# Kernel tuning notes

Measured on AMD Instinct MI355X. Metric: run time of the kernel, lower is better.

## Reference

```python
import jax, jax.numpy as jnp
import numpy as np

VOCAB = 50257
CH = 1024          # c_hidden_size = hidden_size(1020) + class_num(4)
LAT = 128
T = 1024
EOS = 1


def setup_inputs() -> dict:
    key = jax.random.key(0)
    ks = jax.random.split(key, 12)
    s = 0.02
    # tokens in [2, VOCAB) so EOS only appears at the final position
    toks = jax.random.randint(ks[0], (T,), 2, VOCAB, dtype=jnp.int32)
    input_tensor = toks.at[-1].set(EOS)
    inp = {
        "input_tensor": input_tensor,
        "h0": jnp.zeros((1, 1, CH), jnp.float32),
        "c0": jnp.zeros((1, 1, CH), jnp.float32),
        "eps": jax.random.normal(ks[1], (1, 1, LAT), jnp.float32),
        "emb": jax.random.normal(ks[2], (VOCAB, CH), jnp.float32) * s,
        "W_ih": jax.random.normal(ks[3], (4 * CH, CH), jnp.float32) * s,
        "W_hh": jax.random.normal(ks[4], (4 * CH, CH), jnp.float32) * s,
        "b_ih": jax.random.normal(ks[5], (4 * CH,), jnp.float32) * s,
        "b_hh": jax.random.normal(ks[6], (4 * CH,), jnp.float32) * s,
        "W_mean": jax.random.normal(ks[7], (LAT, 2 * CH), jnp.float32) * s,
        "b_mean": jnp.zeros((LAT,), jnp.float32),
        "W_logv": jax.random.normal(ks[8], (LAT, 2 * CH), jnp.float32) * s,
        "b_logv": jnp.zeros((LAT,), jnp.float32),
    }
    return inp


def reference(input_tensor, h0, c0, eps, emb, W_ih, W_hh, b_ih, b_hh,
              W_mean, b_mean, W_logv, b_logv):
    Tlen = input_tensor.shape[0]
    eos_idx = jnp.argmax(input_tensor == EOS)           # first EOS position
    active = jnp.arange(Tlen) < eos_idx                 # steps taken before break
    x_all = emb[input_tensor]                            # [T, CH]

    def step(carry, inp):
        h, c = carry
        x, a = inp
        gates = x @ W_ih.T + b_ih + h @ W_hh.T + b_hh    # [4*CH]
        i, f, g, o = jnp.split(gates, 4)                 # PyTorch LSTM gate order
        c_new = jax.nn.sigmoid(f) * c + jax.nn.sigmoid(i) * jnp.tanh(g)
        h_new = jax.nn.sigmoid(o) * jnp.tanh(c_new)
        h = jnp.where(a, h_new, h)
        c = jnp.where(a, c_new, c)
        return (h, c), None

    (h, c), _ = jax.lax.scan(step, (h0.reshape(-1), c0.reshape(-1)), (x_all, active))
    hc = jnp.concatenate([h, c])                         # cat((h, c), dim=2) flattened
    mean = hc @ W_mean.T + b_mean
    logv = hc @ W_logv.T + b_logv
    z = eps.reshape(-1) * jnp.exp(0.5 * logv) + mean     # reparameterize
    shp = (1, 1, LAT)
    return z.reshape(shp), mean.reshape(shp), logv.reshape(shp)
```

## Files before the change

kernel.cpp:

```cpp
#include <hip/hip_runtime.h>
#include <cstdint>
#include <cstddef>

#define T_LEN 1024
#define CH    1024
#define NGATE 4096
#define LAT   128
#define NBLK  128

#define WS_XG    0
#define WS_HBUF  (16777216)
#define WS_HFIN  (16777216 + 16384)
#define WS_CFIN  (16777216 + 24576)
#define WS_CTRL  (16777216 + 32768)

#define SWZ(i) ((i) ^ ((((i) >> 4) & 7) << 2))

__device__ __forceinline__ float sigmf(float x) { return 1.0f / (1.0f + expf(-x)); }

template <int CTRL, int RM>
__device__ __forceinline__ float dpp_add(float x) {
  int t = __builtin_amdgcn_update_dpp(0, __float_as_int(x), CTRL, RM, 0xf, true);
  return x + __int_as_float(t);
}

__device__ __forceinline__ float wave_sum63(float x) {
  x = dpp_add<0x111, 0xf>(x);
  x = dpp_add<0x112, 0xf>(x);
  x = dpp_add<0x114, 0xf>(x);
  x = dpp_add<0x118, 0xf>(x);
  x = dpp_add<0x142, 0xa>(x);
  x = dpp_add<0x143, 0xc>(x);
  return x;
}

__global__ __launch_bounds__(1024) void setup_k(const int* __restrict__ tok,
                                                int* __restrict__ ctrl) {
  __shared__ int red[1024];
  int tid = threadIdx.x;
  red[tid] = (tok[tid] == 1) ? tid : 0x7fffffff;
  __syncthreads();
  for (int s = 512; s > 0; s >>= 1) {
    if (tid < s) red[tid] = min(red[tid], red[tid + s]);
    __syncthreads();
  }
  if (tid == 0) {
    int e = red[0];
    ctrl[0] = (e == 0x7fffffff) ? 0 : e;
  }
}

__global__ __launch_bounds__(512) void xgemm_k(const int* __restrict__ tok,
                                               const float* __restrict__ emb,
                                               const float* __restrict__ Wih,
                                               const float* __restrict__ bih,
                                               const float* __restrict__ bhh,
                                               float* __restrict__ xg) {
  __shared__ float As[16 * 132];
  __shared__ float Bs[16 * 132];
  const int tid = threadIdx.x;
  const int r0 = blockIdx.x * 128;
  const int t0 = blockIdx.y * 128;
  const int tx = tid & 15, ty = tid >> 4;
  const int m0 = ty * 4, n0 = tx * 8;
  const int lrow = tid >> 2;
  const int kq   = (tid & 3) * 4;

  float acc[4][8];
#pragma unroll
  for (int i = 0; i < 4; i++)
#pragma unroll
    for (int j = 0; j < 8; j++) acc[i][j] = 0.0f;

  const int tokv = tok[t0 + lrow];
  const float* arow = emb + (size_t)tokv * CH;
  const float* brow = Wih + (size_t)(r0 + lrow) * CH;

  for (int k0 = 0; k0 < CH; k0 += 16) {
    float4 a4 = *(const float4*)(arow + k0 + kq);
    float4 b4 = *(const float4*)(brow + k0 + kq);
    __syncthreads();
    As[(kq + 0) * 132 + lrow] = a4.x;
    As[(kq + 1) * 132 + lrow] = a4.y;
    As[(kq + 2) * 132 + lrow] = a4.z;
    As[(kq + 3) * 132 + lrow] = a4.w;
    Bs[(kq + 0) * 132 + lrow] = b4.x;
    Bs[(kq + 1) * 132 + lrow] = b4.y;
    Bs[(kq + 2) * 132 + lrow] = b4.z;
    Bs[(kq + 3) * 132 + lrow] = b4.w;
    __syncthreads();
#pragma unroll
    for (int kk = 0; kk < 16; kk++) {
      float4 av = *(const float4*)&As[kk * 132 + m0];
      float4 b0 = *(const float4*)&Bs[kk * 132 + n0];
      float4 b1 = *(const float4*)&Bs[kk * 132 + n0 + 4];
      float aa[4] = {av.x, av.y, av.z, av.w};
      float bb[8] = {b0.x, b0.y, b0.z, b0.w, b1.x, b1.y, b1.z, b1.w};
#pragma unroll
      for (int i = 0; i < 4; i++)
#pragma unroll
        for (int j = 0; j < 8; j++) acc[i][j] += aa[i] * bb[j];
    }
  }

  float4 bi0 = *(const float4*)(bih + r0 + n0);
  float4 bi1 = *(const float4*)(bih + r0 + n0 + 4);
  float4 bh0 = *(const float4*)(bhh + r0 + n0);
  float4 bh1 = *(const float4*)(bhh + r0 + n0 + 4);
  float badd[8] = {bi0.x + bh0.x, bi0.y + bh0.y, bi0.z + bh0.z, bi0.w + bh0.w,
                   bi1.x + bh1.x, bi1.y + bh1.y, bi1.z + bh1.z, bi1.w + bh1.w};
#pragma unroll
  for (int i = 0; i < 4; i++) {
    float4 o0 = {acc[i][0] + badd[0], acc[i][1] + badd[1],
                 acc[i][2] + badd[2], acc[i][3] + badd[3]};
    float4 o1 = {acc[i][4] + badd[4], acc[i][5] + badd[5],
                 acc[i][6] + badd[6], acc[i][7] + badd[7]};
    float* dst = xg + (size_t)(t0 + m0 + i) * NGATE + r0 + n0;
    *(float4*)(dst) = o0;
    *(float4*)(dst + 4) = o1;
  }
}

__global__ __launch_bounds__(1024) void lstm_k(const float* __restrict__ h0,
                                               const float* __restrict__ c0,
                                               const float* __restrict__ eps,
                                               const float* __restrict__ Whh,
                                               const float* __restrict__ Wm,
                                               const float* __restrict__ bm,
                                               const float* __restrict__ Wl,
                                               const float* __restrict__ bl,
                                               const float* __restrict__ xg,
                                               unsigned long long* __restrict__ hbuf64,
                                               unsigned long long* __restrict__ hfin64,
                                               unsigned long long* __restrict__ cfin64,
                                               const int* __restrict__ ctrl,
                                               float* __restrict__ out) {
  __shared__ float hs[1024];
  __shared__ float hcs[2048];
  __shared__ float4 gpart[16];
  __shared__ float rs[32];

  const int tid = threadIdx.x;
  const int b = blockIdx.x;
  const int wv = tid >> 6;
  const int ln = tid & 63;
  const int dw = wv & 7;
  const int mb = (wv >> 3) * 2;
  const int hsw = SWZ(tid);
  const int swzmask = (ln & 7) << 2;
  const int idx0 = (ln * 16 + 4 * mb) ^ swzmask;
  const int idx1 = (ln * 16 + 4 * mb + 4) ^ swzmask;

  float4 w4[4][2];
#pragma unroll
  for (int q = 0; q < 4; q++) {
    const float* wr = Whh + (size_t)(q * 1024 + b * 8 + dw) * CH + ln * 16 + 4 * mb;
    w4[q][0] = *(const float4*)(wr);
    w4[q][1] = *(const float4*)(wr + 4);
  }

  const int eos = ctrl[0];

  float hreg = 0.0f, creg = 0.0f;
  if (tid < 8) { hreg = h0[b * 8 + tid]; creg = c0[b * 8 + tid]; }

  for (int t = 0; t < eos; t++) {
    float xq0 = 0.0f, xq1 = 0.0f, xq2 = 0.0f, xq3 = 0.0f;
    if (tid < 8) {
      const float* xp = xg + (size_t)t * NGATE + b * 8 + tid;
      xq0 = xp[0]; xq1 = xp[1024]; xq2 = xp[2048]; xq3 = xp[3072];
    }

    if (t == 0) {
      hs[hsw] = h0[tid];
    } else {
      const unsigned want = (unsigned)t;
      const unsigned long long* src = hbuf64 + (size_t)(t & 1) * 1024 + tid;
      unsigned long long v;
      do {
        v = __hip_atomic_load(src, __ATOMIC_RELAXED, __HIP_MEMORY_SCOPE_AGENT);
      } while ((unsigned)(v >> 32) != want);
      hs[hsw] = __uint_as_float((unsigned)(v & 0xffffffffu));
    }
    __syncthreads();

    float a0 = 0.0f, a1 = 0.0f, a2 = 0.0f, a3 = 0.0f;
    {
      const float4 h4a = *(const float4*)&hs[idx0];
      const float4 h4b = *(const float4*)&hs[idx1];
      a0 += w4[0][0].x * h4a.x; a0 += w4[0][0].y * h4a.y;
      a0 += w4[0][0].z * h4a.z; a0 += w4[0][0].w * h4a.w;
      a0 += w4[0][1].x * h4b.x; a0 += w4[0][1].y * h4b.y;
      a0 += w4[0][1].z * h4b.z; a0 += w4[0][1].w * h4b.w;
      a1 += w4[1][0].x * h4a.x; a1 += w4[1][0].y * h4a.y;
      a1 += w4[1][0].z * h4a.z; a1 += w4[1][0].w * h4a.w;
      a1 += w4[1][1].x * h4b.x; a1 += w4[1][1].y * h4b.y;
      a1 += w4[1][1].z * h4b.z; a1 += w4[1][1].w * h4b.w;
      a2 += w4[2][0].x * h4a.x; a2 += w4[2][0].y * h4a.y;
      a2 += w4[2][0].z * h4a.z; a2 += w4[2][0].w * h4a.w;
      a2 += w4[2][1].x * h4b.x; a2 += w4[2][1].y * h4b.y;
      a2 += w4[2][1].z * h4b.z; a2 += w4[2][1].w * h4b.w;
      a3 += w4[3][0].x * h4a.x; a3 += w4[3][0].y * h4a.y;
      a3 += w4[3][0].z * h4a.z; a3 += w4[3][0].w * h4a.w;
      a3 += w4[3][1].x * h4b.x; a3 += w4[3][1].y * h4b.y;
      a3 += w4[3][1].z * h4b.z; a3 += w4[3][1].w * h4b.w;
    }
    a0 = wave_sum63(a0);
    a1 = wave_sum63(a1);
    a2 = wave_sum63(a2);
    a3 = wave_sum63(a3);
    if (ln == 63) gpart[wv] = float4{a0, a1, a2, a3};
    __syncthreads();

    if (tid < 8) {
      const float4 g0 = gpart[tid];
      const float4 g1 = gpart[tid + 8];
      const float iv = g0.x + g1.x + xq0;
      const float fv = g0.y + g1.y + xq1;
      const float gg = g0.z + g1.z + xq2;
      const float ov = g0.w + g1.w + xq3;
      const float cn = sigmf(fv) * creg + sigmf(iv) * tanhf(gg);
      const float hn = sigmf(ov) * tanhf(cn);
      creg = cn; hreg = hn;
      const unsigned long long pv =
          ((unsigned long long)(unsigned)(t + 1) << 32) |
          (unsigned long long)__float_as_uint(hn);
      __hip_atomic_store(&hbuf64[(size_t)((t + 1) & 1) * 1024 + b * 8 + tid], pv,
                         __ATOMIC_RELAXED, __HIP_MEMORY_SCOPE_AGENT);
    }
  }

  if (tid < 8) {
    const unsigned long long ph = (1ull << 32) | (unsigned long long)__float_as_uint(hreg);
    const unsigned long long pc = (1ull << 32) | (unsigned long long)__float_as_uint(creg);
    __hip_atomic_store(&hfin64[b * 8 + tid], ph, __ATOMIC_RELAXED, __HIP_MEMORY_SCOPE_AGENT);
    __hip_atomic_store(&cfin64[b * 8 + tid], pc, __ATOMIC_RELAXED, __HIP_MEMORY_SCOPE_AGENT);
  }

  {
    unsigned long long vh, vc;
    do {
      vh = __hip_atomic_load(&hfin64[tid], __ATOMIC_RELAXED, __HIP_MEMORY_SCOPE_AGENT);
    } while ((unsigned)(vh >> 32) != 1u);
    do {
      vc = __hip_atomic_load(&cfin64[tid], __ATOMIC_RELAXED, __HIP_MEMORY_SCOPE_AGENT);
    } while ((unsigned)(vc >> 32) != 1u);
    hcs[tid] = __uint_as_float((unsigned)(vh & 0xffffffffu));
    hcs[1024 + tid] = __uint_as_float((unsigned)(vc & 0xffffffffu));
  }
  __syncthreads();

  float hc1 = hcs[tid];
  float hc2 = hcs[1024 + tid];
  float pm = Wm[(size_t)b * 2048 + tid] * hc1 + Wm[(size_t)b * 2048 + 1024 + tid] * hc2;
  float pl = Wl[(size_t)b * 2048 + tid] * hc1 + Wl[(size_t)b * 2048 + 1024 + tid] * hc2;
#pragma unroll
  for (int o = 32; o > 0; o >>= 1) {
    pm += __shfl_down(pm, o);
    pl += __shfl_down(pl, o);
  }
  if (ln == 0) { rs[wv] = pm; rs[16 + wv] = pl; }
  __syncthreads();
  if (tid == 0) {
    float m = 0.0f, l = 0.0f;
    for (int i = 0; i < 16; i++) { m += rs[i]; l += rs[16 + i]; }
    m += bm[b];
    l += bl[b];
    float z = eps[b] * expf(0.5f * l) + m;
    out[b] = z;
    out[LAT + b] = m;
    out[2 * LAT + b] = l;
  }
}

extern "C" void kernel_launch(void* const* d_in, const int* in_sizes, int n_in,
                              void* d_out, int out_size, void* d_ws, size_t ws_size,
                              hipStream_t stream) {
  const int*   tok = (const int*)d_in[0];
  const float* h0  = (const float*)d_in[1];
  const float* c0  = (const float*)d_in[2];
  const float* eps = (const float*)d_in[3];
  const float* emb = (const float*)d_in[4];
  const float* Wih = (const float*)d_in[5];
  const float* Whh = (const float*)d_in[6];
  const float* bih = (const float*)d_in[7];
  const float* bhh = (const float*)d_in[8];
  const float* Wm  = (const float*)d_in[9];
  const float* bm  = (const float*)d_in[10];
  const float* Wl  = (const float*)d_in[11];
  const float* bl  = (const float*)d_in[12];
  float* out = (float*)d_out;

  char* ws = (char*)d_ws;
  float* xg = (float*)(ws + WS_XG);
  unsigned long long* hbuf64 = (unsigned long long*)(ws + WS_HBUF);
  unsigned long long* hfin64 = (unsigned long long*)(ws + WS_HFIN);
  unsigned long long* cfin64 = (unsigned long long*)(ws + WS_CFIN);
  int* ctrl = (int*)(ws + WS_CTRL);

  setup_k<<<1, 1024, 0, stream>>>(tok, ctrl);
  xgemm_k<<<dim3(NGATE / 128, T_LEN / 128), 512, 0, stream>>>(tok, emb, Wih, bih, bhh, xg);

  void* args[] = {(void*)&h0, (void*)&c0, (void*)&eps, (void*)&Whh,
                  (void*)&Wm, (void*)&bm, (void*)&Wl, (void*)&bl,
                  (void*)&xg, (void*)&hbuf64, (void*)&hfin64, (void*)&cfin64,
                  (void*)&ctrl, (void*)&out};
  hipLaunchCooperativeKernel((void*)lstm_k, dim3(NBLK), dim3(1024), args, 0, stream);
}
```

Baseline: 2.494 ms.

## Fuse input projection and EOS search into persistent LSTM kernel

Removes the separate EOS-search kernel and the up-front input GEMM over all timesteps. Each block now keeps its slice of W_ih in registers alongside W_hh and computes the input contribution per step from the embedding row, adding biases at the end. This drops two launches and the full precomputed gate buffer, but adds per-step embedding loads and twice the FMA work inside the latency-bound recurrent loop, and doubles weight register pressure. The LDS swizzle pattern is also changed.

```diff
diff --git a/kernel.cpp b/kernel.cpp
--- a/kernel.cpp
+++ b/kernel.cpp
@@ -8,13 +8,11 @@
 #define LAT   128
 #define NBLK  128
 
-#define WS_XG    0
 #define WS_HBUF  (16777216)
 #define WS_HFIN  (16777216 + 16384)
 #define WS_CFIN  (16777216 + 24576)
-#define WS_CTRL  (16777216 + 32768)
-
-#define SWZ(i) ((i) ^ ((((i) >> 4) & 7) << 2))
+
+#define SWZ(j) ((j) ^ ((((j) >> 5) & 7) << 2))
 
 __device__ __forceinline__ float sigmf(float x) { return 1.0f / (1.0f + expf(-x)); }
 
@@ -34,111 +32,28 @@
   return x;
 }
 
-__global__ __launch_bounds__(1024) void setup_k(const int* __restrict__ tok,
-                                                int* __restrict__ ctrl) {
-  __shared__ int red[1024];
-  int tid = threadIdx.x;
-  red[tid] = (tok[tid] == 1) ? tid : 0x7fffffff;
-  __syncthreads();
-  for (int s = 512; s > 0; s >>= 1) {
-    if (tid < s) red[tid] = min(red[tid], red[tid + s]);
-    __syncthreads();
-  }
-  if (tid == 0) {
-    int e = red[0];
-    ctrl[0] = (e == 0x7fffffff) ? 0 : e;
-  }
-}
-
-__global__ __launch_bounds__(512) void xgemm_k(const int* __restrict__ tok,
-                                               const float* __restrict__ emb,
-                                               const float* __restrict__ Wih,
-                                               const float* __restrict__ bih,
-                                               const float* __restrict__ bhh,
-                                               float* __restrict__ xg) {
-  __shared__ float As[16 * 132];
-  __shared__ float Bs[16 * 132];
-  const int tid = threadIdx.x;
-  const int r0 = blockIdx.x * 128;
-  const int t0 = blockIdx.y * 128;
-  const int tx = tid & 15, ty = tid >> 4;
-  const int m0 = ty * 4, n0 = tx * 8;
-  const int lrow = tid >> 2;
-  const int kq   = (tid & 3) * 4;
-
-  float acc[4][8];
-#pragma unroll
-  for (int i = 0; i < 4; i++)
-#pragma unroll
-    for (int j = 0; j < 8; j++) acc[i][j] = 0.0f;
-
-  const int tokv = tok[t0 + lrow];
-  const float* arow = emb + (size_t)tokv * CH;
-  const float* brow = Wih + (size_t)(r0 + lrow) * CH;
-
-  for (int k0 = 0; k0 < CH; k0 += 16) {
-    float4 a4 = *(const float4*)(arow + k0 + kq);
-    float4 b4 = *(const float4*)(brow + k0 + kq);
-    __syncthreads();
-    As[(kq + 0) * 132 + lrow] = a4.x;
-    As[(kq + 1) * 132 + lrow] = a4.y;
-    As[(kq + 2) * 132 + lrow] = a4.z;
-    As[(kq + 3) * 132 + lrow] = a4.w;
-    Bs[(kq + 0) * 132 + lrow] = b4.x;
-    Bs[(kq + 1) * 132 + lrow] = b4.y;
-    Bs[(kq + 2) * 132 + lrow] = b4.z;
-    Bs[(kq + 3) * 132 + lrow] = b4.w;
-    __syncthreads();
-#pragma unroll
-    for (int kk = 0; kk < 16; kk++) {
-      float4 av = *(const float4*)&As[kk * 132 + m0];
-      float4 b0 = *(const float4*)&Bs[kk * 132 + n0];
-      float4 b1 = *(const float4*)&Bs[kk * 132 + n0 + 4];
-      float aa[4] = {av.x, av.y, av.z, av.w};
-      float bb[8] = {b0.x, b0.y, b0.z, b0.w, b1.x, b1.y, b1.z, b1.w};
-#pragma unroll
-      for (int i = 0; i < 4; i++)
-#pragma unroll
-        for (int j = 0; j < 8; j++) acc[i][j] += aa[i] * bb[j];
-    }
-  }
-
-  float4 bi0 = *(const float4*)(bih + r0 + n0);
-  float4 bi1 = *(const float4*)(bih + r0 + n0 + 4);
-  float4 bh0 = *(const float4*)(bhh + r0 + n0);
-  float4 bh1 = *(const float4*)(bhh + r0 + n0 + 4);
-  float badd[8] = {bi0.x + bh0.x, bi0.y + bh0.y, bi0.z + bh0.z, bi0.w + bh0.w,
-                   bi1.x + bh1.x, bi1.y + bh1.y, bi1.z + bh1.z, bi1.w + bh1.w};
-#pragma unroll
-  for (int i = 0; i < 4; i++) {
-    float4 o0 = {acc[i][0] + badd[0], acc[i][1] + badd[1],
-                 acc[i][2] + badd[2], acc[i][3] + badd[3]};
-    float4 o1 = {acc[i][4] + badd[4], acc[i][5] + badd[5],
-                 acc[i][6] + badd[6], acc[i][7] + badd[7]};
-    float* dst = xg + (size_t)(t0 + m0 + i) * NGATE + r0 + n0;
-    *(float4*)(dst) = o0;
-    *(float4*)(dst + 4) = o1;
-  }
-}
-
-__global__ __launch_bounds__(1024) void lstm_k(const float* __restrict__ h0,
-                                               const float* __restrict__ c0,
-                                               const float* __restrict__ eps,
-                                               const float* __restrict__ Whh,
-                                               const float* __restrict__ Wm,
-                                               const float* __restrict__ bm,
-                                               const float* __restrict__ Wl,
-                                               const float* __restrict__ bl,
-                                               const float* __restrict__ xg,
-                                               unsigned long long* __restrict__ hbuf64,
-                                               unsigned long long* __restrict__ hfin64,
-                                               unsigned long long* __restrict__ cfin64,
-                                               const int* __restrict__ ctrl,
-                                               float* __restrict__ out) {
+__global__ __launch_bounds__(1024, 4) void lstm_k(const int* __restrict__ tok,
+                                                  const float* __restrict__ h0,
+                                                  const float* __restrict__ c0,
+                                                  const float* __restrict__ eps,
+                                                  const float* __restrict__ emb,
+                                                  const float* __restrict__ Wih,
+                                                  const float* __restrict__ Whh,
+                                                  const float* __restrict__ bih,
+                                                  const float* __restrict__ bhh,
+                                                  const float* __restrict__ Wm,
+                                                  const float* __restrict__ bm,
+                                                  const float* __restrict__ Wl,
+                                                  const float* __restrict__ bl,
+                                                  unsigned long long* __restrict__ hbuf64,
+                                                  unsigned long long* __restrict__ hfin64,
+                                                  unsigned long long* __restrict__ cfin64,
+                                                  float* __restrict__ out) {
   __shared__ float hs[1024];
   __shared__ float hcs[2048];
   __shared__ float4 gpart[16];
   __shared__ float rs[32];
+  __shared__ int red[1024];
 
   const int tid = threadIdx.x;
   const int b = blockIdx.x;
@@ -146,30 +61,50 @@
   const int ln = tid & 63;
   const int dw = wv & 7;
   const int mb = (wv >> 3) * 2;
+  const int kbase = ln * 16 + 4 * mb;
   const int hsw = SWZ(tid);
-  const int swzmask = (ln & 7) << 2;
-  const int idx0 = (ln * 16 + 4 * mb) ^ swzmask;
-  const int idx1 = (ln * 16 + 4 * mb + 4) ^ swzmask;
+  const int swzmask = ((ln >> 1) & 7) << 2;
+  const int idx0 = kbase ^ swzmask;
+  const int idx1 = (kbase + 4) ^ swzmask;
+
+  red[tid] = (tok[tid] == 1) ? tid : 0x7fffffff;
+  __syncthreads();
+  for (int s = 512; s > 0; s >>= 1) {
+    if (tid < s) red[tid] = min(red[tid], red[tid + s]);
+    __syncthreads();
+  }
+  const int e0 = red[0];
+  const int eos = (e0 == 0x7fffffff) ? 0 : e0;
+  __syncthreads();
 
   float4 w4[4][2];
+  float4 wx[4][2];
 #pragma unroll
   for (int q = 0; q < 4; q++) {
-    const float* wr = Whh + (size_t)(q * 1024 + b * 8 + dw) * CH + ln * 16 + 4 * mb;
-    w4[q][0] = *(const float4*)(wr);
-    w4[q][1] = *(const float4*)(wr + 4);
-  }
-
-  const int eos = ctrl[0];
+    const size_t roff = (size_t)(q * 1024 + b * 8 + dw) * CH + kbase;
+    w4[q][0] = *(const float4*)(Whh + roff);
+    w4[q][1] = *(const float4*)(Whh + roff + 4);
+    wx[q][0] = *(const float4*)(Wih + roff);
+    wx[q][1] = *(const float4*)(Wih + roff + 4);
+  }
+
+  float bias[4] = {0.f, 0.f, 0.f, 0.f};
+  if (tid < 8) {
+#pragma unroll
+    for (int q = 0; q < 4; q++) {
+      const int r = q * 1024 + b * 8 + tid;
+      bias[q] = bih[r] + bhh[r];
+    }
+  }
 
   float hreg = 0.0f, creg = 0.0f;
   if (tid < 8) { hreg = h0[b * 8 + tid]; creg = c0[b * 8 + tid]; }
 
   for (int t = 0; t < eos; t++) {
-    float xq0 = 0.0f, xq1 = 0.0f, xq2 = 0.0f, xq3 = 0.0f;
-    if (tid < 8) {
-      const float* xp = xg + (size_t)t * NGATE + b * 8 + tid;
-      xq0 = xp[0]; xq1 = xp[1024]; xq2 = xp[2048]; xq3 = xp[3072];
-    }
+    const int tokv = tok[t];
+    const float* xrow = emb + (size_t)tokv * CH + kbase;
+    const float4 x4a = *(const float4*)(xrow);
+    const float4 x4b = *(const float4*)(xrow + 4);
 
     if (t == 0) {
       hs[hsw] = h0[tid];
@@ -184,8 +119,24 @@
     }
     __syncthreads();
 
-    float a0 = 0.0f, a1 = 0.0f, a2 = 0.0f, a3 = 0.0f;
+    float a0, a1, a2, a3;
     {
+      a0 = wx[0][0].x * x4a.x + wx[0][0].y * x4a.y +
+           wx[0][0].z * x4a.z + wx[0][0].w * x4a.w +
+           wx[0][1].x * x4b.x + wx[0][1].y * x4b.y +
+           wx[0][1].z * x4b.z + wx[0][1].w * x4b.w;
+      a1 = wx[1][0].x * x4a.x + wx[1][0].y * x4a.y +
+           wx[1][0].z * x4a.z + wx[1][0].w * x4a.w +
+           wx[1][1].x * x4b.x + wx[1][1].y * x4b.y +
+           wx[1][1].z * x4b.z + wx[1][1].w * x4b.w;
+      a2 = wx[2][0].x * x4a.x + wx[2][0].y * x4a.y +
+           wx[2][0].z * x4a.z + wx[2][0].w * x4a.w +
+           wx[2][1].x * x4b.x + wx[2][1].y * x4b.y +
+           wx[2][1].z * x4b.z + wx[2][1].w * x4b.w;
+      a3 = wx[3][0].x * x4a.x + wx[3][0].y * x4a.y +
+           wx[3][0].z * x4a.z + wx[3][0].w * x4a.w +
+           wx[3][1].x * x4b.x + wx[3][1].y * x4b.y +
+           wx[3][1].z * x4b.z + wx[3][1].w * x4b.w;
       const float4 h4a = *(const float4*)&hs[idx0];
       const float4 h4b = *(const float4*)&hs[idx1];
       a0 += w4[0][0].x * h4a.x; a0 += w4[0][0].y * h4a.y;
@@ -215,10 +166,10 @@
     if (tid < 8) {
       const float4 g0 = gpart[tid];
       const float4 g1 = gpart[tid + 8];
-      const float iv = g0.x + g1.x + xq0;
-      const float fv = g0.y + g1.y + xq1;
-      const float gg = g0.z + g1.z + xq2;
-      const float ov = g0.w + g1.w + xq3;
+      const float iv = g0.x + g1.x + bias[0];
+      const float fv = g0.y + g1.y + bias[1];
+      const float gg = g0.z + g1.z + bias[2];
+      const float ov = g0.w + g1.w + bias[3];
       const float cn = sigmf(fv) * creg + sigmf(iv) * tanhf(gg);
       const float hn = sigmf(ov) * tanhf(cn);
       creg = cn; hreg = hn;
@@ -292,18 +243,13 @@
   float* out = (float*)d_out;
 
   char* ws = (char*)d_ws;
-  float* xg = (float*)(ws + WS_XG);
   unsigned long long* hbuf64 = (unsigned long long*)(ws + WS_HBUF);
   unsigned long long* hfin64 = (unsigned long long*)(ws + WS_HFIN);
   unsigned long long* cfin64 = (unsigned long long*)(ws + WS_CFIN);
-  int* ctrl = (int*)(ws + WS_CTRL);
-
-  setup_k<<<1, 1024, 0, stream>>>(tok, ctrl);
-  xgemm_k<<<dim3(NGATE / 128, T_LEN / 128), 512, 0, stream>>>(tok, emb, Wih, bih, bhh, xg);
-
-  void* args[] = {(void*)&h0, (void*)&c0, (void*)&eps, (void*)&Whh,
+
+  void* args[] = {(void*)&tok, (void*)&h0, (void*)&c0, (void*)&eps,
+                  (void*)&emb, (void*)&Wih, (void*)&Whh, (void*)&bih, (void*)&bhh,
                   (void*)&Wm, (void*)&bm, (void*)&Wl, (void*)&bl,
-                  (void*)&xg, (void*)&hbuf64, (void*)&hfin64, (void*)&cfin64,
-                  (void*)&ctrl, (void*)&out};
+                  (void*)&hbuf64, (void*)&hfin64, (void*)&cfin64, (void*)&out};
   hipLaunchCooperativeKernel((void*)lstm_k, dim3(NBLK), dim3(1024), args, 0, stream);
 }
```

Result: faster. 2.363 ms (-5.3%).
